# Optimization experiments

Hardware: AMD Instinct MI355X
Metric: run time of the kernel (lower is better)

Reference implementation:

```python
import jax, jax.numpy as jnp
import numpy as np

THRESHOLD = 8.0
B, C, H, W = 16, 512, 56, 56


def setup_inputs() -> dict:
    key = jax.random.key(0)
    # scale by 3 so per-channel max|x| ~ 13 > threshold -> channels disassemble with T=2
    x = jax.random.normal(key, (B, C, H, W), dtype=jnp.float32) * 3.0
    return {"x": x}


def _plan(x):
    """Host-side plan (mirrors the .item() host sync in the torch module).
    Returns outlier channel ids, the gather index that replicates each outlier
    channel T times, and the matching 1/T scale per output channel."""
    xv = np.asarray(x)
    max_vals = np.max(np.abs(xv), axis=(0, 2, 3))              # [C] per-channel max|x|
    outlier_idx = np.nonzero(max_vals > THRESHOLD)[0]          # channels to disassemble
    T = np.ceil(max_vals[outlier_idx] / THRESHOLD).astype(np.int64)
    rep_idx = np.repeat(outlier_idx, T)                        # each outlier channel repeated T times
    inv_T = np.repeat((1.0 / T).astype(np.float32), T)         # per-output-channel scale 1/T
    return outlier_idx, rep_idx, inv_T


def reference(x):
    outlier_idx, rep_idx, inv_T = _plan(x)
    rep = jnp.asarray(rep_idx)
    scale = jnp.asarray(inv_T)
    # single fused gather + scale replaces the per-channel slice/divide/repeat/concat loop
    disassembled_x = x[:, rep, :, :] * scale[None, :, None, None]
    return disassembled_x, jnp.asarray(outlier_idx)
```

## Files before the change

kernel.cpp:

```cpp
#include <hip/hip_runtime.h>

#define CH    512
#define BATCH 16
#define QB    4
#define NQ    (BATCH / QB)
#define HW    3136
#define HW4   784
#define THRESH 8.0f

typedef float f4 __attribute__((ext_vector_type(4)));

__global__ __launch_bounds__(256) void absmax_kernel(const float* __restrict__ x,
                                                     float* __restrict__ partial) {
    const int c   = blockIdx.x;
    const int q   = blockIdx.y;
    const int tid = threadIdx.x;
    float m = 0.0f;
    for (int bb = 0; bb < QB; ++bb) {
        const int b = q * QB + bb;
        const f4* src = reinterpret_cast<const f4*>(x) + (size_t)(b * CH + c) * HW4;
        for (int p = tid; p < HW4; p += 256) {
            f4 v = src[p];
            m = fmaxf(m, fmaxf(fmaxf(fabsf(v.x), fabsf(v.y)),
                               fmaxf(fabsf(v.z), fabsf(v.w))));
        }
    }
    __shared__ float sm[256];
    sm[tid] = m;
    __syncthreads();
    for (int off = 128; off > 0; off >>= 1) {
        if (tid < off) sm[tid] = fmaxf(sm[tid], sm[tid + off]);
        __syncthreads();
    }
    if (tid == 0) partial[c * NQ + q] = sm[0];
}

__global__ __launch_bounds__(256) void gather_kernel(const float* __restrict__ x,
                                                     const float* __restrict__ partial,
                                                     float* __restrict__ out,
                                                     float* __restrict__ out_tail,
                                                     int R) {
    const int nwg  = gridDim.x;
    const int orig = blockIdx.x;
    const int xcd  = orig & 7;
    const int q8 = nwg >> 3, r8 = nwg & 7;
    const int j = (xcd < r8 ? xcd * (q8 + 1) : r8 * (q8 + 1) + (xcd - r8) * q8)
                  + (orig >> 3);

    const int tid  = threadIdx.x;
    const int lane = tid & 63;
    const int w    = tid >> 6;

    const int c0 = tid * 2, c1 = c0 + 1;
    f4 p0 = reinterpret_cast<const f4*>(partial)[tid * 2];
    f4 p1 = reinterpret_cast<const f4*>(partial)[tid * 2 + 1];
    float m0 = fmaxf(fmaxf(p0.x, p0.y), fmaxf(p0.z, p0.w));
    float m1 = fmaxf(fmaxf(p1.x, p1.y), fmaxf(p1.z, p1.w));
    int T0 = (m0 > THRESH) ? (int)ceilf(m0 * 0.125f) : 0;
    int T1 = (m1 > THRESH) ? (int)ceilf(m1 * 0.125f) : 0;
    const int v = T0 + T1;

    int s = v;
    #pragma unroll
    for (int off = 1; off < 64; off <<= 1) {
        int t2 = __shfl_up(s, off, 64);
        if (lane >= off) s += t2;
    }
    __shared__ int wsum[4];
    if (lane == 63) wsum[w] = s;
    __syncthreads();
    int woff = 0;
    #pragma unroll
    for (int k = 0; k < 4; ++k) if (k < w) woff += wsum[k];
    const int excl   = woff + s - v;
    const int start0 = excl, start1 = excl + T0;

    __shared__ int sc, sT;
    if (T0 > 0 && j >= start0 && j < start0 + T0) { sc = c0; sT = T0; }
    if (T1 > 0 && j >= start1 && j < start1 + T1) { sc = c1; sT = T1; }

    if (j == 0) {
        const int o0 = (T0 > 0), o1 = (T1 > 0);
        const int v2 = o0 + o1;
        int s2 = v2;
        #pragma unroll
        for (int off = 1; off < 64; off <<= 1) {
            int t2 = __shfl_up(s2, off, 64);
            if (lane >= off) s2 += t2;
        }
        __shared__ int wsum2[4];
        if (lane == 63) wsum2[w] = s2;
        __syncthreads();
        int woff2 = 0;
        #pragma unroll
        for (int k = 0; k < 4; ++k) if (k < w) woff2 += wsum2[k];
        const int ex2 = woff2 + s2 - v2;
        if (o0) out_tail[ex2]      = (float)c0;
        if (o1) out_tail[ex2 + o0] = (float)c1;
    }
    __syncthreads();

    const int   c     = sc;
    const float scale = (float)(1.0 / (double)sT);

    const f4* srcb = reinterpret_cast<const f4*>(x)   + (size_t)c * HW4;
    f4*       dstb = reinterpret_cast<f4*>(out)       + (size_t)j * HW4;
    for (int idx = tid; idx < BATCH * HW4; idx += 256) {
        const int b = idx / HW4;
        f4 vv = srcb[(size_t)b * (CH * HW4 - HW4) + idx];
        vv.x *= scale; vv.y *= scale; vv.z *= scale; vv.w *= scale;
        __builtin_nontemporal_store(vv, &dstb[(size_t)b * ((size_t)(R - 1) * HW4) + idx]);
    }
}

extern "C" void kernel_launch(void* const* d_in, const int* in_sizes, int n_in,
                              void* d_out, int out_size, void* d_ws, size_t ws_size,
                              hipStream_t stream) {
    const float* x = (const float*)d_in[0];
    float* out = (float*)d_out;

    const int plane = BATCH * HW;
    const int R     = out_size / plane;

    float* partial = (float*)d_ws;

    absmax_kernel<<<dim3(CH, NQ), 256, 0, stream>>>(x, partial);
    if (R > 0) {
        gather_kernel<<<dim3(R), 256, 0, stream>>>(
            x, partial, out, out + (size_t)R * plane, R);
    }
}
```

Baseline: 65.36 us.

## Fuse absmax and gather kernels with atomic-counter grid barrier

Merges the per-channel absmax reduction and the replicated gather into one persistent-style kernel of 2048 blocks. Each block first computes one partial max, then bumps one of 64 striped atomic counters. Blocks with index below R spin on the counters until all partials are published, then do the gather. This removes a second kernel launch and the gap between kernels, at the cost of a memset launch, spin-wait traffic and a deadlock risk if not all blocks are co-resident. The bounded guard that breaks out of the spin could also let a block read incomplete partials.

```diff
diff --git a/kernel.cpp b/kernel.cpp
--- a/kernel.cpp
+++ b/kernel.cpp
@@ -2,58 +2,75 @@
 
 #define CH    512
 #define BATCH 16
-#define QB    4
-#define NQ    (BATCH / QB)
 #define HW    3136
 #define HW4   784
 #define THRESH 8.0f
+#define NBLK  2048
+#define NCNT  64
+#define CNT_TARGET 32u
 
 typedef float f4 __attribute__((ext_vector_type(4)));
 
-__global__ __launch_bounds__(256) void absmax_kernel(const float* __restrict__ x,
-                                                     float* __restrict__ partial) {
-    const int c   = blockIdx.x;
-    const int q   = blockIdx.y;
-    const int tid = threadIdx.x;
-    float m = 0.0f;
-    for (int bb = 0; bb < QB; ++bb) {
-        const int b = q * QB + bb;
-        const f4* src = reinterpret_cast<const f4*>(x) + (size_t)(b * CH + c) * HW4;
-        for (int p = tid; p < HW4; p += 256) {
-            f4 v = src[p];
-            m = fmaxf(m, fmaxf(fmaxf(fabsf(v.x), fabsf(v.y)),
-                               fmaxf(fabsf(v.z), fabsf(v.w))));
+__global__ __launch_bounds__(256, 8) void fused_kernel(
+        const float*  __restrict__ x,
+        float*        __restrict__ partial,
+        unsigned int* __restrict__ cnt,
+        float*        __restrict__ out,
+        float*        __restrict__ out_tail,
+        int R) {
+    const int w    = blockIdx.x;
+    const int tid  = threadIdx.x;
+    const int lane = tid & 63;
+    const int wv   = tid >> 6;
+
+    {
+        const int c = w & (CH - 1);
+        const int q = w >> 9;
+        float m = 0.0f;
+        for (int bb = 0; bb < 4; ++bb) {
+            const int b = q * 4 + bb;
+            const f4* src = reinterpret_cast<const f4*>(x) + (size_t)(b * CH + c) * HW4;
+            for (int p = tid; p < HW4; p += 256) {
+                f4 v = src[p];
+                m = fmaxf(m, fmaxf(fmaxf(fabsf(v.x), fabsf(v.y)),
+                                   fmaxf(fabsf(v.z), fabsf(v.w))));
+            }
+        }
+        __shared__ float sm[256];
+        sm[tid] = m;
+        __syncthreads();
+        for (int off = 128; off > 0; off >>= 1) {
+            if (tid < off) sm[tid] = fmaxf(sm[tid], sm[tid + off]);
+            __syncthreads();
+        }
+        if (tid == 0) {
+            partial[c * 4 + q] = sm[0];
+            __hip_atomic_fetch_add(&cnt[w & (NCNT - 1)], 1u,
+                                   __ATOMIC_RELEASE, __HIP_MEMORY_SCOPE_AGENT);
         }
     }
-    __shared__ float sm[256];
-    sm[tid] = m;
+
+    if (w >= R) return;
+
+    if (tid < NCNT) {
+        int guard = 0;
+        while (__hip_atomic_load(&cnt[tid], __ATOMIC_ACQUIRE,
+                                 __HIP_MEMORY_SCOPE_AGENT) < CNT_TARGET) {
+            __builtin_amdgcn_s_sleep(2);
+            if (++guard > (1 << 20)) break;
+        }
+    }
     __syncthreads();
-    for (int off = 128; off > 0; off >>= 1) {
-        if (tid < off) sm[tid] = fmaxf(sm[tid], sm[tid + off]);
-        __syncthreads();
-    }
-    if (tid == 0) partial[c * NQ + q] = sm[0];
-}
 
-__global__ __launch_bounds__(256) void gather_kernel(const float* __restrict__ x,
-                                                     const float* __restrict__ partial,
-                                                     float* __restrict__ out,
-                                                     float* __restrict__ out_tail,
-                                                     int R) {
-    const int nwg  = gridDim.x;
-    const int orig = blockIdx.x;
-    const int xcd  = orig & 7;
+    const int nwg = R;
+    const int xcd = w & 7;
     const int q8 = nwg >> 3, r8 = nwg & 7;
     const int j = (xcd < r8 ? xcd * (q8 + 1) : r8 * (q8 + 1) + (xcd - r8) * q8)
-                  + (orig >> 3);
-
-    const int tid  = threadIdx.x;
-    const int lane = tid & 63;
-    const int w    = tid >> 6;
+                  + (w >> 3);
 
     const int c0 = tid * 2, c1 = c0 + 1;
-    f4 p0 = reinterpret_cast<const f4*>(partial)[tid * 2];
-    f4 p1 = reinterpret_cast<const f4*>(partial)[tid * 2 + 1];
+    f4 p0 = reinterpret_cast<const f4*>(partial)[c0];
+    f4 p1 = reinterpret_cast<const f4*>(partial)[c1];
     float m0 = fmaxf(fmaxf(p0.x, p0.y), fmaxf(p0.z, p0.w));
     float m1 = fmaxf(fmaxf(p1.x, p1.y), fmaxf(p1.z, p1.w));
     int T0 = (m0 > THRESH) ? (int)ceilf(m0 * 0.125f) : 0;
@@ -67,11 +84,11 @@
         if (lane >= off) s += t2;
     }
     __shared__ int wsum[4];
-    if (lane == 63) wsum[w] = s;
+    if (lane == 63) wsum[wv] = s;
     __syncthreads();
     int woff = 0;
     #pragma unroll
-    for (int k = 0; k < 4; ++k) if (k < w) woff += wsum[k];
+    for (int k = 0; k < 4; ++k) if (k < wv) woff += wsum[k];
     const int excl   = woff + s - v;
     const int start0 = excl, start1 = excl + T0;
 
@@ -89,11 +106,11 @@
             if (lane >= off) s2 += t2;
         }
         __shared__ int wsum2[4];
-        if (lane == 63) wsum2[w] = s2;
+        if (lane == 63) wsum2[wv] = s2;
         __syncthreads();
         int woff2 = 0;
         #pragma unroll
-        for (int k = 0; k < 4; ++k) if (k < w) woff2 += wsum2[k];
+        for (int k = 0; k < 4; ++k) if (k < wv) woff2 += wsum2[k];
         const int ex2 = woff2 + s2 - v2;
         if (o0) out_tail[ex2]      = (float)c0;
         if (o1) out_tail[ex2 + o0] = (float)c1;
@@ -122,11 +139,10 @@
     const int plane = BATCH * HW;
     const int R     = out_size / plane;
 
-    float* partial = (float*)d_ws;
+    float*        partial = (float*)d_ws;
+    unsigned int* cnt     = (unsigned int*)((char*)d_ws + 8192);
 
-    absmax_kernel<<<dim3(CH, NQ), 256, 0, stream>>>(x, partial);
-    if (R > 0) {
-        gather_kernel<<<dim3(R), 256, 0, stream>>>(
-            x, partial, out, out + (size_t)R * plane, R);
-    }
+    hipMemsetAsync(cnt, 0, NCNT * sizeof(unsigned int), stream);
+    fused_kernel<<<dim3(NBLK), 256, 0, stream>>>(
+        x, partial, cnt, out, out + (size_t)R * plane, R);
 }
```

Result: slower. 151.0 us (+131.0%).
